# Kernel tuning notes

Measured on AMD Instinct MI355X. Metric: run time of the kernel, lower is better.

Reference implementation:

```python
import jax, jax.numpy as jnp
import numpy as np

B, T, D, H = 128, 512, 64, 256  # batch, n_target, input_size, hidden_size

def setup_inputs() -> dict:
    key = jax.random.key(0)
    ks = jax.random.split(key, 12)
    sc_ih = 1.0 / np.sqrt(H)
    return {
        "x_input": jax.random.normal(ks[0], (B, T * D), dtype=jnp.float32),
        "h0": jax.random.normal(ks[1], (1, B, H), dtype=jnp.float32) * 0.1,
        "c0": jax.random.normal(ks[2], (1, B, H), dtype=jnp.float32) * 0.1,
        "W_ih": jax.random.normal(ks[3], (4 * H, D), dtype=jnp.float32) * sc_ih,
        "W_hh": jax.random.normal(ks[4], (4 * H, H), dtype=jnp.float32) * sc_ih,
        "b_ih": jax.random.normal(ks[5], (4 * H,), dtype=jnp.float32) * sc_ih,
        "b_hh": jax.random.normal(ks[6], (4 * H,), dtype=jnp.float32) * sc_ih,
        "f1_w": jax.random.normal(ks[7], (128, H), dtype=jnp.float32) * sc_ih,
        "f1_b": jax.random.normal(ks[8], (128,), dtype=jnp.float32) * sc_ih,
        "f2_w": jax.random.normal(ks[9], (128, H), dtype=jnp.float32) * sc_ih,
        "f2_b": jax.random.normal(ks[10], (128,), dtype=jnp.float32) * sc_ih,
        "long": 10,
    }

def reference(x_input, h0, c0, W_ih, W_hh, b_ih, b_hh, f1_w, f1_b, f2_w, f2_b, long):
    b = x_input.shape[0]
    d = W_ih.shape[1]
    state = x_input.reshape(b, -1, d)            # (B, T, D)
    t = state.shape[1]
    h_prev, c_prev = h0[0], c0[0]                # (B, H) shared initial state for every step
    # All single-step LSTM calls are independent -> one batched GEMM over (B, T)
    gates = (jnp.einsum('btd,gd->btg', state, W_ih) + b_ih
             + (h_prev @ W_hh.T + b_hh)[:, None, :])         # (B, T, 4H)
    i_g, f_g, g_g, o_g = jnp.split(gates, 4, axis=-1)        # torch gate order: i, f, g, o
    i_g = jax.nn.sigmoid(i_g); f_g = jax.nn.sigmoid(f_g)
    g_g = jnp.tanh(g_g);       o_g = jax.nn.sigmoid(o_g)
    c_all = f_g * c_prev[:, None, :] + i_g * g_g             # (B, T, H)
    h_all = o_g * jnp.tanh(c_all)
    # original loop starts at i=1, so step 0 keeps zero hidden/cell
    mask = (jnp.arange(t) > 0).astype(x_input.dtype)[None, :, None]
    h_all = h_all * mask
    c_all = c_all * mask
    w0 = state[:, :, 0] / long                               # (B, T)
    w1 = state[:, :, 1]
    def agg(v):
        a = jnp.einsum('bth,kh->btk', v, f1_w) + f1_b        # f1 per step
        bb = jnp.einsum('bth,kh->btk', v, f2_w) + f2_b       # f2 per step
        first = jnp.einsum('btk,bt->bk', a, w0)              # weighted sum over t
        second = jnp.einsum('btk,bt->bk', bb, w1)
        return jnp.concatenate([first, second], axis=-1)[None]  # (1, B, 256)
    return (agg(h_all), agg(c_all))
```

## Files before the change

### kernel.cpp

```cpp
#include <hip/hip_runtime.h>

#define BDIM 128
#define TDIM 512
#define DDIM 64
#define HDIM 256
#define BH    (BDIM * HDIM)
#define W_OFF (4 * BH)
#define HH_OFF (W_OFF + 256)

typedef short s16x8 __attribute__((ext_vector_type(8)));
typedef float f32x4 __attribute__((ext_vector_type(4)));

#if __has_builtin(__builtin_amdgcn_exp2f)
#define EXP2(x) __builtin_amdgcn_exp2f(x)
#else
#define EXP2(x) exp2f(x)
#endif
#define L2E 1.44269504f

__device__ __forceinline__ float rcpf(float x) { return __builtin_amdgcn_rcpf(x); }

__device__ __forceinline__ short f2bf(float f) {
  __bf16 b = (__bf16)f;
  return __builtin_bit_cast(short, b);
}

__device__ __forceinline__ s16x8 pack_bf8(float4 lo, float4 hi) {
  s16x8 v;
  v[0] = f2bf(lo.x); v[1] = f2bf(lo.y); v[2] = f2bf(lo.z); v[3] = f2bf(lo.w);
  v[4] = f2bf(hi.x); v[5] = f2bf(hi.y); v[6] = f2bf(hi.z); v[7] = f2bf(hi.w);
  return v;
}

__device__ __forceinline__ s16x8 pack_bf8s(float4 lo, float4 hi, float s) {
  s16x8 v;
  v[0] = f2bf(lo.x*s); v[1] = f2bf(lo.y*s); v[2] = f2bf(lo.z*s); v[3] = f2bf(lo.w*s);
  v[4] = f2bf(hi.x*s); v[5] = f2bf(hi.y*s); v[6] = f2bf(hi.z*s); v[7] = f2bf(hi.w*s);
  return v;
}

__global__ __launch_bounds__(256) void hh_mfma_kernel(
    const float* __restrict__ h0, const float* __restrict__ Whh,
    const float* __restrict__ bih, const float* __restrict__ bhh,
    const float* __restrict__ x, const int* __restrict__ longp,
    float* __restrict__ sbuf)
{
  const int bt   = blockIdx.x;
  const int nt   = blockIdx.y;
  const int tid  = threadIdx.x;
  const int wave = tid >> 6;
  const int lane = tid & 63;
  const int col  = lane & 15;
  const int kg   = lane >> 4;
  const int b0   = bt * 16;

  if (nt == 16) {
    const int bl = tid >> 4, part = tid & 15;
    const int b = b0 + bl;
    const float* xb = x + (size_t)b * (TDIM * DDIM);
    const float inv_long = 1.0f / (float)(*longp);
    float sa = 0.f, sb = 0.f;
    for (int t = part; t < TDIM; t += 16) {
      float2 v = *(const float2*)(xb + (size_t)t * DDIM);
      sa += v.x; sb += v.y;
    }
    #pragma unroll
    for (int off = 1; off < 16; off <<= 1) {
      sa += __shfl_xor(sa, off, 64);
      sb += __shfl_xor(sb, off, 64);
    }
    if (part == 0) {
      sbuf[W_OFF + b * 2 + 0] = sa * inv_long;
      sbuf[W_OFF + b * 2 + 1] = sb;
    }
    return;
  }

  const int colw = nt * 64 + wave * 16 + col;
  const float bias = bih[colw] + bhh[colw];

  const float* arow = h0  + (size_t)(b0 + col) * HDIM + kg * 8;
  const float* brow = Whh + (size_t)colw * HDIM + kg * 8;

  f32x4 acc = {0.f, 0.f, 0.f, 0.f};
  #pragma unroll
  for (int s = 0; s < 8; ++s) {
    float4 a0 = *(const float4*)(arow + s * 32);
    float4 a1 = *(const float4*)(arow + s * 32 + 4);
    float4 q0 = *(const float4*)(brow + s * 32);
    float4 q1 = *(const float4*)(brow + s * 32 + 4);
    acc = __builtin_amdgcn_mfma_f32_16x16x32_bf16(
        pack_bf8(a0, a1), pack_bf8(q0, q1), acc, 0, 0, 0);
  }

  float* hh = sbuf + HH_OFF;
  #pragma unroll
  for (int r = 0; r < 4; ++r) {
    const int m = kg * 4 + r;
    hh[(size_t)(b0 + m) * 1024 + colw] = acc[r] + bias;
  }
}

__global__ __launch_bounds__(512, 4) void fused_lstm(
    const float* __restrict__ x, const float* __restrict__ c0,
    const float* __restrict__ Wih, const int* __restrict__ longp,
    float* __restrict__ sbuf)
{
  const int b    = blockIdx.x;
  const int hcq  = blockIdx.y;
  const int tid  = threadIdx.x;
  const int wave = tid >> 6;
  const int lane = tid & 63;
  const int col  = lane & 15;
  const int kg   = lane >> 4;
  const int hp   = wave & 3;
  const int tq   = wave >> 2;
  const int h    = hcq * 64 + hp * 16 + col;

  __shared__ float red[8 * 64];

  const float* hh = sbuf + HH_OFF;
  const float* xb = x + (size_t)b * (TDIM * DDIM);
  const float inv_long = 1.0f / (float)(*longp);

  const float SC[4] = {L2E, L2E, 2.f * L2E, L2E};
  float hhv[4];
  #pragma unroll
  for (int g = 0; g < 4; ++g)
    hhv[g] = hh[(size_t)b * 1024 + g * HDIM + h] * SC[g];
  const float cprev = c0[b * HDIM + h];

  s16x8 wf[4][2];
  #pragma unroll
  for (int g = 0; g < 4; ++g) {
    const float4* wrow = (const float4*)(Wih + (size_t)(g * HDIM + h) * DDIM);
    #pragma unroll
    for (int ks = 0; ks < 2; ++ks)
      wf[g][ks] = pack_bf8s(wrow[kg * 2 + ks * 8], wrow[kg * 2 + ks * 8 + 1], SC[g]);
  }

  const int t0w = tq * 256;
  const float* arow = xb + (size_t)(t0w + col) * DDIM + kg * 8;

  float4 nxt0 = *(const float4*)(arow + 0);
  float4 nxt1 = *(const float4*)(arow + 4);
  float4 nxt2 = *(const float4*)(arow + 32);
  float4 nxt3 = *(const float4*)(arow + 36);
  s16x8 a0 = pack_bf8(nxt0, nxt1);
  s16x8 a1 = pack_bf8(nxt2, nxt3);
  float w0c = nxt0.x, w1c = nxt0.y;
  if (tq == 0 && lane == 0) { w0c = 0.f; w1c = 0.f; }

  float s0h = 0.f, s1h = 0.f, s0c = 0.f, s1c = 0.f;

  for (int tb = 0; tb < 256; tb += 16) {
    const bool has_next = (tb + 16) < 256;
    if (has_next) {
      const float* p = arow + (size_t)(tb + 16) * DDIM;
      nxt0 = *(const float4*)(p + 0);
      nxt1 = *(const float4*)(p + 4);
      nxt2 = *(const float4*)(p + 32);
      nxt3 = *(const float4*)(p + 36);
    }

    f32x4 acc[4];
    #pragma unroll
    for (int g = 0; g < 4; ++g) {
      f32x4 zc = {hhv[g], hhv[g], hhv[g], hhv[g]};
      zc = __builtin_amdgcn_mfma_f32_16x16x32_bf16(a0, wf[g][0], zc, 0, 0, 0);
      zc = __builtin_amdgcn_mfma_f32_16x16x32_bf16(a1, wf[g][1], zc, 0, 0, 0);
      acc[g] = zc;
    }

    #pragma unroll
    for (int r = 0; r < 4; ++r) {
      float wx = __shfl(w0c, kg * 4 + r, 64);
      float wy = __shfl(w1c, kg * 4 + r, 64);
      float eA = EXP2(-acc[0][r]);
      float eC = EXP2(-acc[1][r]);
      float eB = EXP2( acc[2][r]);
      float eD = EXP2(-acc[3][r]);
      float igg = (eB - 1.f) * rcpf((1.f + eA) * (eB + 1.f));
      float fg  = rcpf(1.f + eC);
      float cc  = fmaf(fg, cprev, igg);
      float eE  = EXP2(cc * (2.f * L2E));
      float hv  = (eE - 1.f) * rcpf((1.f + eD) * (eE + 1.f));
      s0h = fmaf(hv, wx, s0h); s1h = fmaf(hv, wy, s1h);
      s0c = fmaf(cc, wx, s0c); s1c = fmaf(cc, wy, s1c);
    }

    if (has_next) {
      a0 = pack_bf8(nxt0, nxt1);
      a1 = pack_bf8(nxt2, nxt3);
      w0c = nxt0.x; w1c = nxt0.y;
    }
  }

  s0h += __shfl_xor(s0h, 16, 64); s0h += __shfl_xor(s0h, 32, 64);
  s1h += __shfl_xor(s1h, 16, 64); s1h += __shfl_xor(s1h, 32, 64);
  s0c += __shfl_xor(s0c, 16, 64); s0c += __shfl_xor(s0c, 32, 64);
  s1c += __shfl_xor(s1c, 16, 64); s1c += __shfl_xor(s1c, 32, 64);

  if (kg == 0) {
    red[wave * 64 +  0 + col] = s0h * inv_long;
    red[wave * 64 + 16 + col] = s1h;
    red[wave * 64 + 32 + col] = s0c * inv_long;
    red[wave * 64 + 48 + col] = s1c;
  }
  __syncthreads();

  if (tid < 256) {
    const int hp2 = tid >> 6;
    const int q   = (tid >> 4) & 3;
    const int cc2 = tid & 15;
    const int o   = q * 16 + cc2;
    float s = red[hp2 * 64 + o] + red[(4 + hp2) * 64 + o];
    const int h2 = hcq * 64 + hp2 * 16 + cc2;
    sbuf[(size_t)q * BH + b * HDIM + h2] = s;
  }
}

__global__ __launch_bounds__(256) void out_mfma_kernel(
    const float* __restrict__ f1w, const float* __restrict__ f1b,
    const float* __restrict__ f2w, const float* __restrict__ f2b,
    const float* __restrict__ sbuf, float* __restrict__ out)
{
  const int bt   = blockIdx.x;
  const int kt   = blockIdx.y;
  const int tid  = threadIdx.x;
  const int wave = tid >> 6;
  const int lane = tid & 63;
  const int col  = lane & 15;
  const int kg   = lane >> 4;
  const int b0   = bt * 16;
  const int k0   = kt * 16;

  const int q        = (wave == 0) ? 0 : (wave == 1) ? 2 : (wave == 2) ? 1 : 3;
  const float* Wm    = (wave < 2) ? f1w : f2w;
  const float* bv    = (wave < 2) ? f1b : f2b;
  const int   kout   = (wave < 2) ? k0 : (128 + k0);
  const int   opl    = (wave & 1);
  const int   wsel   = (wave < 2) ? 0 : 1;

  const float* arow = sbuf + (size_t)q * BH + (size_t)(b0 + col) * HDIM + kg * 8;
  const float* brow = Wm + (size_t)(k0 + col) * HDIM + kg * 8;

  f32x4 acc = {0.f, 0.f, 0.f, 0.f};
  #pragma unroll
  for (int s = 0; s < 8; ++s) {
    float4 a0 = *(const float4*)(arow + s * 32);
    float4 a1 = *(const float4*)(arow + s * 32 + 4);
    float4 q0 = *(const float4*)(brow + s * 32);
    float4 q1 = *(const float4*)(brow + s * 32 + 4);
    acc = __builtin_amdgcn_mfma_f32_16x16x32_bf16(
        pack_bf8(a0, a1), pack_bf8(q0, q1), acc, 0, 0, 0);
  }

  const float bw = bv[k0 + col];
  #pragma unroll
  for (int r = 0; r < 4; ++r) {
    const int b = b0 + kg * 4 + r;
    const float Wv = sbuf[W_OFF + b * 2 + wsel];
    out[(size_t)opl * BH + (size_t)b * HDIM + kout + col] = acc[r] + bw * Wv;
  }
}

extern "C" void kernel_launch(void* const* d_in, const int* in_sizes, int n_in,
                              void* d_out, int out_size, void* d_ws, size_t ws_size,
                              hipStream_t stream) {
  const float* x   = (const float*)d_in[0];
  const float* h0  = (const float*)d_in[1];
  const float* c0  = (const float*)d_in[2];
  const float* Wih = (const float*)d_in[3];
  const float* Whh = (const float*)d_in[4];
  const float* bih = (const float*)d_in[5];
  const float* bhh = (const float*)d_in[6];
  const float* f1w = (const float*)d_in[7];
  const float* f1b = (const float*)d_in[8];
  const float* f2w = (const float*)d_in[9];
  const float* f2b = (const float*)d_in[10];
  const int*  longp = (const int*)d_in[11];
  float* out  = (float*)d_out;
  float* sbuf = (float*)d_ws;

  dim3 gh(8, 17);
  hh_mfma_kernel<<<gh, 256, 0, stream>>>(h0, Whh, bih, bhh, x, longp, sbuf);
  dim3 g1(BDIM, 4);
  fused_lstm<<<g1, 512, 0, stream>>>(x, c0, Wih, longp, sbuf);
  dim3 go(8, 8);
  out_mfma_kernel<<<go, 256, 0, stream>>>(f1w, f1b, f2w, f2b, sbuf, out);
}
```

Before: 59.22 us.

## Fuse output projection into LSTM kernel via last-block atomic counter

Removes the separate output MFMA kernel. Each batch row now gets an atomic counter, reset in the first kernel. The last of the four h-chunk blocks for a row computes the f1/f2 projections for that row with scalar FP32 dot products. This saves a kernel launch and its gap, at the cost of threadfences, an atomic per block, and a serial, less parallel tail GEMV done in the last block.

After: 147.6 us. +149.2%, slower.

```diff
diff --git a/kernel.cpp b/kernel.cpp
--- a/kernel.cpp
+++ b/kernel.cpp
@@ -7,6 +7,7 @@
 #define BH    (BDIM * HDIM)
 #define W_OFF (4 * BH)
 #define HH_OFF (W_OFF + 256)
+#define CNT_OFF (HH_OFF + BDIM * 1024)
 
 typedef short s16x8 __attribute__((ext_vector_type(8)));
 typedef float f32x4 __attribute__((ext_vector_type(4)));
@@ -55,6 +56,8 @@
   const int b0   = bt * 16;
 
   if (nt == 16) {
+    if (bt == 0 && tid < BDIM)
+      ((int*)(sbuf + CNT_OFF))[tid] = 0;
     const int bl = tid >> 4, part = tid & 15;
     const int b = b0 + bl;
     const float* xb = x + (size_t)b * (TDIM * DDIM);
@@ -103,8 +106,10 @@
 
 __global__ __launch_bounds__(512, 4) void fused_lstm(
     const float* __restrict__ x, const float* __restrict__ c0,
-    const float* __restrict__ Wih, const int* __restrict__ longp,
-    float* __restrict__ sbuf)
+    const float* __restrict__ Wih, const float* __restrict__ f1w,
+    const float* __restrict__ f1b, const float* __restrict__ f2w,
+    const float* __restrict__ f2b, const int* __restrict__ longp,
+    float* __restrict__ sbuf, float* __restrict__ out)
 {
   const int b    = blockIdx.x;
   const int hcq  = blockIdx.y;
@@ -118,6 +123,7 @@
   const int h    = hcq * 64 + hp * 16 + col;
 
   __shared__ float red[8 * 64];
+  __shared__ int is_last;
 
   const float* hh = sbuf + HH_OFF;
   const float* xb = x + (size_t)b * (TDIM * DDIM);
@@ -218,50 +224,36 @@
     const int h2 = hcq * 64 + hp2 * 16 + cc2;
     sbuf[(size_t)q * BH + b * HDIM + h2] = s;
   }
-}
-
-__global__ __launch_bounds__(256) void out_mfma_kernel(
-    const float* __restrict__ f1w, const float* __restrict__ f1b,
-    const float* __restrict__ f2w, const float* __restrict__ f2b,
-    const float* __restrict__ sbuf, float* __restrict__ out)
-{
-  const int bt   = blockIdx.x;
-  const int kt   = blockIdx.y;
-  const int tid  = threadIdx.x;
-  const int wave = tid >> 6;
-  const int lane = tid & 63;
-  const int col  = lane & 15;
-  const int kg   = lane >> 4;
-  const int b0   = bt * 16;
-  const int k0   = kt * 16;
-
-  const int q        = (wave == 0) ? 0 : (wave == 1) ? 2 : (wave == 2) ? 1 : 3;
-  const float* Wm    = (wave < 2) ? f1w : f2w;
-  const float* bv    = (wave < 2) ? f1b : f2b;
-  const int   kout   = (wave < 2) ? k0 : (128 + k0);
-  const int   opl    = (wave & 1);
-  const int   wsel   = (wave < 2) ? 0 : 1;
-
-  const float* arow = sbuf + (size_t)q * BH + (size_t)(b0 + col) * HDIM + kg * 8;
-  const float* brow = Wm + (size_t)(k0 + col) * HDIM + kg * 8;
-
-  f32x4 acc = {0.f, 0.f, 0.f, 0.f};
-  #pragma unroll
-  for (int s = 0; s < 8; ++s) {
-    float4 a0 = *(const float4*)(arow + s * 32);
-    float4 a1 = *(const float4*)(arow + s * 32 + 4);
-    float4 q0 = *(const float4*)(brow + s * 32);
-    float4 q1 = *(const float4*)(brow + s * 32 + 4);
-    acc = __builtin_amdgcn_mfma_f32_16x16x32_bf16(
-        pack_bf8(a0, a1), pack_bf8(q0, q1), acc, 0, 0, 0);
-  }
-
-  const float bw = bv[k0 + col];
-  #pragma unroll
-  for (int r = 0; r < 4; ++r) {
-    const int b = b0 + kg * 4 + r;
-    const float Wv = sbuf[W_OFF + b * 2 + wsel];
-    out[(size_t)opl * BH + (size_t)b * HDIM + kout + col] = acc[r] + bw * Wv;
+
+  __threadfence();
+  if (tid == 0) {
+    int* cnt = (int*)(sbuf + CNT_OFF);
+    int old = atomicAdd(&cnt[b], 1);
+    is_last = (old == 3);
+  }
+  __syncthreads();
+  if (!is_last) return;
+  __threadfence();
+
+  {
+    const int k    = tid & 255;
+    const int half = tid >> 8;
+    const bool first = (k < 128);
+    const float* Wm = first ? (f1w + (size_t)k * HDIM)
+                            : (f2w + (size_t)(k - 128) * HDIM);
+    const int q = first ? (half ? 2 : 0) : (half ? 3 : 1);
+    const float* pl = sbuf + (size_t)q * BH + (size_t)b * HDIM;
+
+    float acc = 0.f;
+    #pragma unroll 8
+    for (int kk = 0; kk < HDIM / 4; ++kk) {
+      float4 w = *(const float4*)(Wm + kk * 4);
+      float4 p = *(const float4*)(pl + kk * 4);
+      acc += w.x * p.x + w.y * p.y + w.z * p.z + w.w * p.w;
+    }
+    const float Wv = sbuf[W_OFF + b * 2 + (first ? 0 : 1)];
+    const float bb = first ? f1b[k] : f2b[k - 128];
+    out[(size_t)half * BH + (size_t)b * HDIM + k] = acc + bb * Wv;
   }
 }
 
@@ -286,7 +278,6 @@
   dim3 gh(8, 17);
   hh_mfma_kernel<<<gh, 256, 0, stream>>>(h0, Whh, bih, bhh, x, longp, sbuf);
   dim3 g1(BDIM, 4);
-  fused_lstm<<<g1, 512, 0, stream>>>(x, c0, Wih, longp, sbuf);
-  dim3 go(8, 8);
-  out_mfma_kernel<<<go, 256, 0, stream>>>(f1w, f1b, f2w, f2b, sbuf, out);
-}
+  fused_lstm<<<g1, 512, 0, stream>>>(x, c0, Wih, f1w, f1b, f2w, f2b,
+                                     longp, sbuf, out);
+}
```
